# Kernel tuning notes

Hardware: AMD Instinct MI355X
Metric: run time of the kernel (lower is better)

Reference implementation:

```python
import jax, jax.numpy as jnp
import numpy as np

NUM_RELATIONS = 3
NUM_HEADS = 1

N_NODES = 50000
N_EDGES = 300000
D = 256  # in_channels == out_channels == out_channels*num_heads
W_SCALE = 0.02  # realistic init scale; keeps linear-attention normalizer dominated by N_r


def setup_inputs() -> dict:
    key = jax.random.key(0)
    k = jax.random.split(key, 7)
    x = jax.random.normal(k[0], (N_NODES, D), dtype=jnp.float32)
    Wq = jax.random.normal(k[1], (NUM_RELATIONS, D, D * NUM_HEADS), dtype=jnp.float32) * W_SCALE
    Wk = jax.random.normal(k[2], (NUM_RELATIONS, D, D * NUM_HEADS), dtype=jnp.float32) * W_SCALE
    Wv = jax.random.normal(k[3], (NUM_RELATIONS, D, D * NUM_HEADS), dtype=jnp.float32) * W_SCALE
    Whp = jax.random.normal(k[4], (D * NUM_HEADS, D), dtype=jnp.float32) * W_SCALE
    edge_index = jax.random.randint(k[5], (2, N_EDGES), 0, N_NODES, dtype=jnp.int64)
    edge_type = jax.random.randint(k[6], (N_EDGES,), 0, NUM_RELATIONS, dtype=jnp.int64)
    return {"x": x, "Wq": Wq, "Wk": Wk, "Wv": Wv, "Whp": Whp,
            "edge_index": edge_index, "edge_type": edge_type}


def _trans_conv(x, Wq, Wk, Wv, Whp, edge_index, edge_type):
    # x: [N, F], Wq/Wk/Wv: [R, F, H*Dh], Whp: [H*Dh, Dh], edge_index: [2, E]
    row, col = edge_index[0], edge_index[1]
    N = x.shape[0]
    R = Wq.shape[0]
    H = NUM_HEADS
    Dh = Wq.shape[-1] // H
    xr = x[row]  # [E, F] gathered source-node features
    xc = x[col]  # [E, F] gathered target-node features
    x_out = jnp.zeros((N, Dh), dtype=x.dtype)
    for r in range(R):  # small fixed relation loop (structurally distinct weights)
        m = (edge_type == r).astype(x.dtype)  # [E] relation mask (handles ragged sizes)
        Nr = jnp.sum(m)  # number of edges of this relation (the 'N' in full_attention_conv)
        q = (xr @ Wq[r]).reshape(-1, H, Dh)  # [E, H, Dh]
        kk = (xc @ Wk[r]).reshape(-1, H, Dh)
        v = (xc @ Wv[r]).reshape(-1, H, Dh)
        # linear attention (no softmax), masked so only relation-r edges contribute
        kvs = jnp.einsum('e,ehm,ehd->hmd', m, kk, v)        # [H, Dh, Dh]
        num = jnp.einsum('ehm,hmd->ehd', q, kvs) + Nr * v    # [E, H, Dh]
        ks_sum = jnp.einsum('e,ehm->hm', m, kk)              # [H, Dh]
        norm = jnp.einsum('ehm,hm->eh', q, ks_sum)[..., None] + Nr  # [E, H, 1]
        attn = (num / norm).mean(axis=1)                     # [E, Dh] (mean over heads)
        x_out = x_out.at[row].add(m[:, None] * attn)         # scatter-add to source nodes
    return x_out @ Whp  # head projection


def reference(x, Wq, Wk, Wv, Whp, edge_index, edge_type):
    return _trans_conv(x, Wq, Wk, Wv, Whp, edge_index, edge_type)
```

## Files before the change

### kernel.cpp

```cpp
#include <hip/hip_runtime.h>

#define NN 50000
#define EE 300000
#define DD 256
#define RR 3
#define NPAD 50048
#define GS 64
#define SCT (RR * NN)
#define SCB 1024
#define SNB ((SCT + SCB - 1) / SCB)

using bf16x8 = __attribute__((ext_vector_type(8))) short;
using f32x4  = __attribute__((ext_vector_type(4))) float;

__device__ __forceinline__ float bf2f(unsigned short u) {
    return __uint_as_float(((unsigned)u) << 16);
}
__device__ __forceinline__ unsigned short f2bf(float f) {
    unsigned u = __float_as_uint(f);
    return (unsigned short)((u + 0x7fffu + ((u >> 16) & 1u)) >> 16);
}
__device__ __forceinline__ void gload_lds16(const void* g, void* l) {
    __builtin_amdgcn_global_load_lds(
        (const __attribute__((address_space(1))) unsigned int*)g,
        (__attribute__((address_space(3))) unsigned int*)l, 16, 0, 0);
}

__global__ __launch_bounds__(256) void prep_w(
    const float* __restrict__ Wq, const float* __restrict__ Wk,
    const float* __restrict__ Wv, const float* __restrict__ Whp,
    unsigned short* __restrict__ WvTcat, unsigned short* __restrict__ WkT,
    unsigned short* __restrict__ Wqb, unsigned short* __restrict__ WhpT,
    unsigned short* __restrict__ BfullT)
{
    int t = blockIdx.x * 256 + threadIdx.x;
    int slot = t >> 16, o = t & 65535;
    int a = o >> 8, b = o & 255;
    if (slot < 9) {
        int r = slot / 3, kind = slot % 3;
        if (kind == 0)      WvTcat[(size_t)a * 768 + r * 256 + b] = f2bf(Wv[(size_t)r * 65536 + b * 256 + a]);
        else if (kind == 1) WkT[(size_t)r * 65536 + o] = f2bf(Wk[(size_t)r * 65536 + b * 256 + a]);
        else                Wqb[(size_t)r * 65536 + o] = f2bf(Wq[(size_t)r * 65536 + a * 256 + b]);
    } else if (slot == 9) {
        WhpT[o] = f2bf(Whp[b * 256 + a]);
    } else if (slot < 13) {
        int r = slot - 10;
        BfullT[(size_t)768 * 256 + (size_t)r * 65536 + o] = f2bf(Wv[(size_t)r * 65536 + o]);
    }
}

__global__ __launch_bounds__(256) void transpose_conv(
    const float* __restrict__ x, unsigned short* __restrict__ xb,
    unsigned short* __restrict__ xT)
{
    __shared__ unsigned short t[64][66];
    const int n0 = blockIdx.x * 64, i0 = blockIdx.y * 64;
    const int tid = threadIdx.x;
    const int nl = tid >> 2, c0 = (tid & 3) * 16;
    unsigned short vb[16];
    int n = n0 + nl;
    if (n < NN) {
        const float* src = x + (size_t)n * DD + i0 + c0;
#pragma unroll
        for (int q = 0; q < 16; q += 4) {
            float4 v = *(const float4*)(src + q);
            vb[q] = f2bf(v.x); vb[q + 1] = f2bf(v.y);
            vb[q + 2] = f2bf(v.z); vb[q + 3] = f2bf(v.w);
        }
#pragma unroll
        for (int q = 0; q < 16; q += 4)
            *(ushort4*)(xb + (size_t)n * DD + i0 + c0 + q) =
                make_ushort4(vb[q], vb[q + 1], vb[q + 2], vb[q + 3]);
    } else {
#pragma unroll
        for (int q = 0; q < 16; q++) vb[q] = 0;
    }
#pragma unroll
    for (int q = 0; q < 16; q++) t[nl][c0 + q] = vb[q];
    __syncthreads();
    const int il = tid >> 2, nc0 = (tid & 3) * 16;
    unsigned short ob[16];
#pragma unroll
    for (int q = 0; q < 16; q++) ob[q] = t[nc0 + q][il];
#pragma unroll
    for (int q = 0; q < 16; q += 4)
        *(ushort4*)(xT + (size_t)(i0 + il) * NPAD + n0 + nc0 + q) =
            make_ushort4(ob[q], ob[q + 1], ob[q + 2], ob[q + 3]);
}

__global__ __launch_bounds__(256) void count_kernel(
    const int* __restrict__ erow, const int* __restrict__ ecol,
    const int* __restrict__ etype, int* __restrict__ c_in,
    int* __restrict__ c_out, int* __restrict__ nr)
{
    __shared__ int lnr[RR];
    if (threadIdx.x < RR) lnr[threadIdx.x] = 0;
    __syncthreads();
    int g = blockIdx.x * blockDim.x + threadIdx.x;
    int stride = gridDim.x * blockDim.x;
    for (int e = g; e < EE; e += stride) {
        int t = etype[e];
        atomicAdd(&c_out[t * NN + erow[e]], 1);
        atomicAdd(&c_in[t * NN + ecol[e]], 1);
        atomicAdd(&lnr[t], 1);
    }
    __syncthreads();
    if (threadIdx.x < RR) atomicAdd(&nr[threadIdx.x], lnr[threadIdx.x]);
}

__global__ __launch_bounds__(256) void scan_reduce(
    const int* __restrict__ cnt, int* __restrict__ bsum)
{
    __shared__ int ws[4];
    const int b = blockIdx.x, tid = threadIdx.x;
    const int i = b * SCB + tid * 4;
    int s = 0;
    if (i < SCT) {
        int4 v = *(const int4*)(cnt + i);
        s = v.x + v.y + v.z + v.w;
    }
#pragma unroll
    for (int off = 32; off; off >>= 1) s += __shfl_down(s, off, 64);
    if ((tid & 63) == 0) ws[tid >> 6] = s;
    __syncthreads();
    if (tid == 0) bsum[b] = ws[0] + ws[1] + ws[2] + ws[3];
}

__global__ __launch_bounds__(256) void scan_top(
    const int* __restrict__ bsum, int* __restrict__ boff, int* __restrict__ offT)
{
    __shared__ int bs[256];
    const int tid = threadIdx.x;
    int v = tid < SNB ? bsum[tid] : 0;
    bs[tid] = v;
    __syncthreads();
    for (int d = 1; d < 256; d <<= 1) {
        int t = (tid >= d) ? bs[tid - d] : 0;
        __syncthreads();
        bs[tid] += t;
        __syncthreads();
    }
    if (tid < SNB) boff[tid] = tid ? bs[tid - 1] : 0;
    if (tid == 255) *offT = bs[255];
}

__global__ __launch_bounds__(256) void scan_bot(
    const int* __restrict__ cnt, const int* __restrict__ boff,
    int* __restrict__ off, int* __restrict__ cur)
{
    __shared__ int bs[256];
    const int b = blockIdx.x, tid = threadIdx.x;
    const int i = b * SCB + tid * 4;
    int4 v = make_int4(0, 0, 0, 0);
    if (i < SCT) v = *(const int4*)(cnt + i);
    int s = v.x + v.y + v.z + v.w;
    bs[tid] = s;
    __syncthreads();
    for (int d = 1; d < 256; d <<= 1) {
        int t = (tid >= d) ? bs[tid - d] : 0;
        __syncthreads();
        bs[tid] += t;
        __syncthreads();
    }
    if (i < SCT) {
        int pre = boff[b] + (tid ? bs[tid - 1] : 0);
        int4 o;
        o.x = pre;
        o.y = pre + v.x;
        o.z = pre + v.x + v.y;
        o.w = pre + v.x + v.y + v.z;
        *(int4*)(off + i) = o;
        *(int4*)(cur + i) = o;
    }
}

__global__ __launch_bounds__(256) void fill_kernel(
    const int* __restrict__ erow, const int* __restrict__ ecol,
    const int* __restrict__ etype, int* __restrict__ cur,
    int* __restrict__ scol)
{
    int e = blockIdx.x * 256 + threadIdx.x;
    if (e < EE) {
        int key = etype[e] * NN + erow[e];
        int p = atomicAdd(&cur[key], 1);
        scol[p] = ecol[e];
    }
}

__global__ __launch_bounds__(256) void gather_kernel(
    const unsigned short* __restrict__ xb, const int* __restrict__ scol,
    const int* __restrict__ off, const float* __restrict__ qs,
    const int* __restrict__ c_out, const int* __restrict__ nr,
    unsigned short* __restrict__ Afull)
{
    const int wid = threadIdx.x >> 6, lane = threadIdx.x & 63;
    const int n = blockIdx.x * 4 + wid;
    if (n >= NN) return;
    ushort4 xv = *(const ushort4*)(xb + (size_t)n * DD + lane * 4);
    float xf[4] = {bf2f(xv.x), bf2f(xv.y), bf2f(xv.z), bf2f(xv.w)};
#pragma unroll
    for (int t = 0; t < RR; t++) {
        float nrf = (float)nr[t];
        float denom = qs[(size_t)t * NN + n] + nrf;
        int cnt = c_out[t * NN + n];
        float s2 = cnt ? (float)cnt / denom : 0.f;
        ushort4 o1;
        o1.x = f2bf(s2 * xf[0]); o1.y = f2bf(s2 * xf[1]);
        o1.z = f2bf(s2 * xf[2]); o1.w = f2bf(s2 * xf[3]);
        *(ushort4*)(Afull + (size_t)n * 1536 + t * 256 + lane * 4) = o1;

        float acc[4] = {0.f, 0.f, 0.f, 0.f};
        int b0 = off[t * NN + n], b1 = off[t * NN + n + 1];
        for (int i = b0; i < b1; i++) {
            int col = scol[i];
            ushort4 v = *(const ushort4*)(xb + (size_t)col * DD + lane * 4);
            acc[0] += bf2f(v.x); acc[1] += bf2f(v.y);
            acc[2] += bf2f(v.z); acc[3] += bf2f(v.w);
        }
        float s1 = nrf / denom;
        ushort4 o2;
        o2.x = f2bf(s1 * acc[0]); o2.y = f2bf(s1 * acc[1]);
        o2.z = f2bf(s1 * acc[2]); o2.w = f2bf(s1 * acc[3]);
        *(ushort4*)(Afull + (size_t)n * 1536 + 768 + t * 256 + lane * 4) = o2;
    }
}

__global__ __launch_bounds__(256) void wbf_kernel(
    const int* __restrict__ c_in, unsigned short* __restrict__ wbf)
{
    int t = blockIdx.x * 256 + threadIdx.x;
    if (t < 3 * NPAD) {
        int r = t / NPAD, n = t % NPAD;
        wbf[t] = f2bf(n < NN ? (float)c_in[r * NN + n] : 0.f);
    }
}

__global__ __launch_bounds__(256) void xw_kernel(
    const unsigned short* __restrict__ xT, const int* __restrict__ c_in,
    float* __restrict__ xw)
{
    __shared__ float red[3][4];
    const int i = blockIdx.x;
    const int tid = threadIdx.x;
    float a0 = 0.f, a1 = 0.f, a2 = 0.f;
    for (int n = tid * 4; n < NN; n += 1024) {
        ushort4 xv = *(const ushort4*)(xT + (size_t)i * NPAD + n);
        int4 w0 = *(const int4*)(c_in + n);
        int4 w1 = *(const int4*)(c_in + NN + n);
        int4 w2 = *(const int4*)(c_in + 2 * NN + n);
        float f0 = bf2f(xv.x), f1 = bf2f(xv.y), f2 = bf2f(xv.z), f3 = bf2f(xv.w);
        a0 += f0 * w0.x + f1 * w0.y + f2 * w0.z + f3 * w0.w;
        a1 += f0 * w1.x + f1 * w1.y + f2 * w1.z + f3 * w1.w;
        a2 += f0 * w2.x + f1 * w2.y + f2 * w2.z + f3 * w2.w;
    }
#pragma unroll
    for (int off = 32; off; off >>= 1) {
        a0 += __shfl_down(a0, off, 64);
        a1 += __shfl_down(a1, off, 64);
        a2 += __shfl_down(a2, off, 64);
    }
    if ((tid & 63) == 0) {
        red[0][tid >> 6] = a0; red[1][tid >> 6] = a1; red[2][tid >> 6] = a2;
    }
    __syncthreads();
    if (tid < 3)
        xw[tid * 256 + i] = red[tid][0] + red[tid][1] + red[tid][2] + red[tid][3];
}

__global__ __launch_bounds__(512) void g_kernel(
    const unsigned short* __restrict__ xT, const unsigned short* __restrict__ wbf,
    float* __restrict__ Gp)
{
    __shared__ __align__(16) char ldsA[16384];
    __shared__ __align__(16) char ldsB[16384];
    const int tid = threadIdx.x, lane = tid & 63, wid = tid >> 6;
    const int wr = wid >> 1, wc = wid & 1;
    const int i0 = blockIdx.x * 128, j0 = blockIdx.y * 128;
    const int TPZ = (NPAD / 64 + GS - 1) / GS;
    const int kt0 = blockIdx.z * TPZ;
    const int kt1 = min(NPAD / 64, kt0 + TPZ);

    f32x4 acc[3][2][4];
#pragma unroll
    for (int r = 0; r < 3; r++)
#pragma unroll
        for (int m = 0; m < 2; m++)
#pragma unroll
            for (int n = 0; n < 4; n++) acc[r][m][n] = (f32x4){0.f, 0.f, 0.f, 0.f};

    for (int kt = kt0; kt < kt1; kt++) {
        const int kbyte = kt * 128;
#pragma unroll
        for (int is = 0; is < 2; is++) {
            int lb = is * 8192 + wid * 1024;
            int d = lb + lane * 16;
            int row = d >> 7;
            int sc_ = (d & 127) ^ ((row & 7) << 4);
            gload_lds16((const char*)xT + (size_t)(i0 + row) * (NPAD * 2) + kbyte + sc_, ldsA + lb);
            gload_lds16((const char*)xT + (size_t)(j0 + row) * (NPAD * 2) + kbyte + sc_, ldsB + lb);
        }
        __syncthreads();
#pragma unroll
        for (int kk = 0; kk < 2; kk++) {
            const int cb = kk * 64 + ((lane >> 4) << 4);
            bf16x8 bfr[4];
#pragma unroll
            for (int n = 0; n < 4; n++) {
                int rn = wc * 64 + n * 16 + (lane & 15);
                bfr[n] = *(const bf16x8*)(ldsB + rn * 128 + (cb ^ ((rn & 7) << 4)));
            }
            float au[2][8];
#pragma unroll
            for (int m = 0; m < 2; m++) {
                int row = wr * 32 + m * 16 + (lane & 15);
                bf16x8 ar = *(const bf16x8*)(ldsA + row * 128 + (cb ^ ((row & 7) << 4)));
#pragma unroll
                for (int q = 0; q < 8; q++) au[m][q] = bf2f((unsigned short)ar[q]);
            }
            const int nb = kt * 64 + kk * 32 + ((lane >> 4) << 3);
#pragma unroll
            for (int r = 0; r < 3; r++) {
                bf16x8 wv = *(const bf16x8*)(wbf + (size_t)r * NPAD + nb);
                float wf[8];
#pragma unroll
                for (int q = 0; q < 8; q++) wf[q] = bf2f((unsigned short)wv[q]);
                bf16x8 am[2];
#pragma unroll
                for (int m = 0; m < 2; m++)
#pragma unroll
                    for (int q = 0; q < 8; q++)
                        am[m][q] = (short)f2bf(au[m][q] * wf[q]);
#pragma unroll
                for (int m = 0; m < 2; m++)
#pragma unroll
                    for (int n = 0; n < 4; n++)
                        acc[r][m][n] = __builtin_amdgcn_mfma_f32_16x16x32_bf16(
                            am[m], bfr[n], acc[r][m][n], 0, 0, 0);
            }
        }
        __syncthreads();
    }
    float* base = Gp + ((size_t)blockIdx.z * 4 + blockIdx.x * 2 + blockIdx.y) * 3 * 16384;
#pragma unroll
    for (int r = 0; r < 3; r++)
#pragma unroll
        for (int m = 0; m < 2; m++)
#pragma unroll
            for (int n = 0; n < 4; n++) {
                int col = wc * 64 + n * 16 + (lane & 15);
                int rw0 = wr * 32 + m * 16 + ((lane >> 4) << 2);
#pragma unroll
                for (int reg = 0; reg < 4; reg++)
                    base[r * 16384 + (rw0 + reg) * 128 + col] = acc[r][m][n][reg];
            }
}

__global__ __launch_bounds__(256) void greduce_kernel(
    const float* __restrict__ Gp, unsigned short* __restrict__ Gb)
{
    int gid = blockIdx.x * 256 + threadIdx.x;
    int t = gid >> 14, rem = gid & 16383;
    int r = t % 3, tile = t / 3;
    float s = 0.f;
    for (int z = 0; z < GS; z++)
        s += Gp[(size_t)z * 196608 + ((size_t)tile * 3 + r) * 16384 + rem];
    int i = (tile >> 1) * 128 + (rem >> 7);
    int j = (tile & 1) * 128 + (rem & 127);
    Gb[(size_t)r * 65536 + i * 256 + j] = f2bf(s);
}

__global__ __launch_bounds__(256) void matvec_bf(
    const unsigned short* __restrict__ Mat, const float* __restrict__ v,
    float* __restrict__ y)
{
    __shared__ float vs[256];
    const int b = blockIdx.x;
    const int r = b >> 6, rb = (b & 63) * 4;
    const int tid = threadIdx.x;
    vs[tid] = v[r * 256 + tid];
    __syncthreads();
    const int wid = tid >> 6, lane = tid & 63;
    const int row = rb + wid;
    ushort4 m4 = *(const ushort4*)(Mat + (size_t)r * 65536 + row * 256 + lane * 4);
    float s = bf2f(m4.x) * vs[lane * 4] + bf2f(m4.y) * vs[lane * 4 + 1] +
              bf2f(m4.z) * vs[lane * 4 + 2] + bf2f(m4.w) * vs[lane * 4 + 3];
#pragma unroll
    for (int off = 32; off; off >>= 1) s += __shfl_down(s, off, 64);
    if (lane == 0) y[r * 256 + row] = s;
}

__global__ __launch_bounds__(256) void qs_kernel(
    const unsigned short* __restrict__ xb, const float* __restrict__ tv,
    float* __restrict__ qs)
{
    __shared__ float ts[768];
    const int tid = threadIdx.x;
    for (int k = tid; k < 768; k += 256) ts[k] = tv[k];
    __syncthreads();
    const int wid = tid >> 6, lane = tid & 63;
    const int n = blockIdx.x * 4 + wid;
    if (n < NN) {
        ushort4 xv = *(const ushort4*)(xb + (size_t)n * DD + lane * 4);
        float xf[4] = {bf2f(xv.x), bf2f(xv.y), bf2f(xv.z), bf2f(xv.w)};
        float s0 = 0, s1 = 0, s2 = 0;
#pragma unroll
        for (int c = 0; c < 4; c++) {
            s0 += xf[c] * ts[lane * 4 + c];
            s1 += xf[c] * ts[256 + lane * 4 + c];
            s2 += xf[c] * ts[512 + lane * 4 + c];
        }
#pragma unroll
        for (int off = 32; off; off >>= 1) {
            s0 += __shfl_down(s0, off, 64);
            s1 += __shfl_down(s1, off, 64);
            s2 += __shfl_down(s2, off, 64);
        }
        if (lane == 0) { qs[n] = s0; qs[NN + n] = s1; qs[2 * NN + n] = s2; }
    }
}

template <int MODE>
__global__ __launch_bounds__(256) void gemm_nt(
    const unsigned short* __restrict__ A, int lda,
    const unsigned short* __restrict__ B, int ldb,
    void* __restrict__ Cv, int ldc, int M, int KK,
    size_t sa, size_t sb, size_t sc)
{
    A += (size_t)blockIdx.z * sa;
    B += (size_t)blockIdx.z * sb;
    __shared__ __align__(16) char ldsA[16384];
    __shared__ __align__(16) char ldsB[16384];
    const int tid = threadIdx.x, lane = tid & 63, wid = tid >> 6;
    const int wr = wid >> 1, wc = wid & 1;
    const int row0 = blockIdx.x * 128, col0 = blockIdx.y * 128;

    f32x4 acc[4][4];
#pragma unroll
    for (int m = 0; m < 4; m++)
#pragma unroll
        for (int n = 0; n < 4; n++) acc[m][n] = (f32x4){0.f, 0.f, 0.f, 0.f};

    for (int k0 = 0; k0 < KK; k0 += 64) {
#pragma unroll
        for (int is = 0; is < 4; is++) {
            int lb = is * 4096 + wid * 1024;
            int d = lb + lane * 16;
            int row = d >> 7;
            int sc_ = (d & 127) ^ ((row & 7) << 4);
            int gr = row0 + row; gr = gr < M ? gr : M - 1;
            gload_lds16((const char*)(A + (size_t)gr * lda + k0) + sc_, ldsA + lb);
            int rn = col0 + row;
            gload_lds16((const char*)(B + (size_t)rn * ldb + k0) + sc_, ldsB + lb);
        }
        __syncthreads();
#pragma unroll
        for (int kk = 0; kk < 2; kk++) {
            bf16x8 af[4], bf_[4];
            const int cb = kk * 64 + ((lane >> 4) << 4);
#pragma unroll
            for (int m = 0; m < 4; m++) {
                int row = wr * 64 + m * 16 + (lane & 15);
                af[m] = *(const bf16x8*)(ldsA + row * 128 + (cb ^ ((row & 7) << 4)));
                int rn = wc * 64 + m * 16 + (lane & 15);
                bf_[m] = *(const bf16x8*)(ldsB + rn * 128 + (cb ^ ((rn & 7) << 4)));
            }
#pragma unroll
            for (int m = 0; m < 4; m++)
#pragma unroll
                for (int n = 0; n < 4; n++)
                    acc[m][n] = __builtin_amdgcn_mfma_f32_16x16x32_bf16(
                        af[m], bf_[n], acc[m][n], 0, 0, 0);
        }
        __syncthreads();
    }

#pragma unroll
    for (int m = 0; m < 4; m++) {
#pragma unroll
        for (int reg = 0; reg < 4; reg++) {
            int r = row0 + wr * 64 + m * 16 + ((lane >> 4) << 2) + reg;
            if (r >= M) continue;
#pragma unroll
            for (int n = 0; n < 4; n++) {
                int c = col0 + wc * 64 + n * 16 + (lane & 15);
                float v = acc[m][n][reg];
                if (MODE == 0)
                    ((unsigned short*)Cv)[(size_t)blockIdx.z * sc + (size_t)r * ldc + c] = f2bf(v);
                else
                    ((float*)Cv)[(size_t)blockIdx.z * sc + (size_t)r * ldc + c] = v;
            }
        }
    }
}

extern "C" void kernel_launch(void* const* d_in, const int* in_sizes, int n_in,
                              void* d_out, int out_size, void* d_ws, size_t ws_size,
                              hipStream_t stream)
{
    const float* x   = (const float*)d_in[0];
    const float* Wq  = (const float*)d_in[1];
    const float* Wk  = (const float*)d_in[2];
    const float* Wv  = (const float*)d_in[3];
    const float* Whp = (const float*)d_in[4];
    const int* eidx  = (const int*)d_in[5];
    const int* etyp  = (const int*)d_in[6];
    const int* erow = eidx;
    const int* ecol = eidx + EE;
    float* out = (float*)d_out;

    char* p = (char*)d_ws;
    unsigned short* xb    = (unsigned short*)p; p += (size_t)NN * DD * 2;
    unsigned short* xT    = (unsigned short*)p; p += (size_t)DD * NPAD * 2;
    char*           regB  = p;                  p += (size_t)NN * 1536 * 2;
    unsigned short* Gb    = (unsigned short*)p; p += (size_t)RR * 65536 * 2;
    unsigned short* U1    = (unsigned short*)p; p += (size_t)RR * 65536 * 2;
    unsigned short* U2    = (unsigned short*)p; p += (size_t)RR * 65536 * 2;
    unsigned short* BfullT= (unsigned short*)p; p += (size_t)1536 * 256 * 2;
    unsigned short* Bout  = (unsigned short*)p; p += (size_t)256 * 1536 * 2;
    unsigned short* WvTcat= (unsigned short*)p; p += (size_t)256 * 768 * 2;
    unsigned short* WkT   = (unsigned short*)p; p += (size_t)RR * 65536 * 2;
    unsigned short* Wqb   = (unsigned short*)p; p += (size_t)RR * 65536 * 2;
    unsigned short* WhpT  = (unsigned short*)p; p += 65536 * 2;
    unsigned short* wbf   = (unsigned short*)p; p += (size_t)RR * NPAD * 2;
    float*          qs    = (float*)p;          p += (size_t)RR * NN * 4;
    float*          xw    = (float*)p;          p += 768 * 4;
    float*          ks    = (float*)p;          p += 768 * 4;
    float*          tv    = (float*)p;          p += 768 * 4;
    int*            c_in  = (int*)p;            p += (size_t)RR * NN * 4;
    int*            c_out = (int*)p;            p += (size_t)RR * NN * 4;
    int*            off   = (int*)p;            p += (size_t)(RR * NN + 4) * 4;
    int*            cur   = (int*)p;            p += (size_t)RR * NN * 4;
    int*            scol  = (int*)p;            p += (size_t)EE * 4;
    int*            nr    = (int*)p;            p += RR * 4;
    int*            bsum  = (int*)p;            p += SNB * 4;
    int*            boff  = (int*)p;            p += SNB * 4;
    float*          Gp    = (float*)regB;
    unsigned short* Afull = (unsigned short*)regB;

    prep_w<<<3328, 256, 0, stream>>>(Wq, Wk, Wv, Whp, WvTcat, WkT, Wqb, WhpT, BfullT);
    transpose_conv<<<dim3(NPAD / 64, 4), 256, 0, stream>>>(x, xb, xT);
    hipMemsetAsync(c_in, 0, (size_t)(6 * NN) * sizeof(int), stream);
    hipMemsetAsync(nr, 0, RR * sizeof(int), stream);
    count_kernel<<<512, 256, 0, stream>>>(erow, ecol, etyp, c_in, c_out, nr);
    scan_reduce<<<SNB, 256, 0, stream>>>(c_out, bsum);
    scan_top<<<1, 256, 0, stream>>>(bsum, boff, off + SCT);
    scan_bot<<<SNB, 256, 0, stream>>>(c_out, boff, off, cur);
    fill_kernel<<<(EE + 255) / 256, 256, 0, stream>>>(erow, ecol, etyp, cur, scol);
    wbf_kernel<<<(3 * NPAD + 255) / 256, 256, 0, stream>>>(c_in, wbf);
    xw_kernel<<<256, 256, 0, stream>>>(xT, c_in, xw);

    g_kernel<<<dim3(2, 2, GS), 512, 0, stream>>>(xT, wbf, Gp);
    greduce_kernel<<<12 * 64, 256, 0, stream>>>(Gp, Gb);

    gemm_nt<0><<<dim3(2, 2, 3), 256, 0, stream>>>(WvTcat, 768, Gb, 256, U1, 256, 256, 256,
                                                  256, 65536, 65536);
    gemm_nt<0><<<dim3(2, 2, 3), 256, 0, stream>>>(U1, 256, WkT, 256, U2, 256, 256, 256,
                                                  65536, 65536, 65536);
    gemm_nt<0><<<dim3(2, 2, 3), 256, 0, stream>>>(Wqb, 256, U2, 256, BfullT, 256, 256, 256,
                                                  65536, 65536, 65536);
    gemm_nt<0><<<dim3(2, 12), 256, 0, stream>>>(WhpT, 256, BfullT, 256, Bout, 1536, 256, 256,
                                                0, 0, 0);
    matvec_bf<<<192, 256, 0, stream>>>(WkT, xw, ks);
    matvec_bf<<<192, 256, 0, stream>>>(Wqb, ks, tv);
    qs_kernel<<<(NN + 3) / 4, 256, 0, stream>>>(xb, tv, qs);

    gather_kernel<<<(NN + 3) / 4, 256, 0, stream>>>(xb, scol, off, qs, c_out, nr, Afull);

    const int MB = (NN + 127) / 128;
    gemm_nt<1><<<dim3(MB, 2), 256, 0, stream>>>(Afull, 1536, Bout, 1536, out, 256, NN, 1536,
                                                0, 0, 0);
}
```

Before: 341.1 us.

## Fuse prep kernels, reassociate small weight GEMM chain, fold qs into gather, swizzle GEMM

Merges weight conversion and x transpose/convert into one launch, and merges the wbf and xw kernels. It reassociates the small weight-product chain: Wq·Wk^T is formed once and reused for both the Gram-based term and the normalizer vector, dropping one 256x256 GEMM and one matvec. It also folds the per-node qs dot products into the gather kernel, removing a kernel and the qs buffer round trip. The final big GEMM gets an XCD-aware block swizzle for better L2 locality. Together these cut launch count and small serial kernels, but the reordered bf16 intermediate products may change rounding.

```diff
diff --git a/kernel.cpp b/kernel.cpp
--- a/kernel.cpp
+++ b/kernel.cpp
@@ -9,6 +9,7 @@
 #define SCT (RR * NN)
 #define SCB 1024
 #define SNB ((SCT + SCB - 1) / SCB)
+#define TBLK 3128
 
 using bf16x8 = __attribute__((ext_vector_type(8))) short;
 using f32x4  = __attribute__((ext_vector_type(4))) float;
@@ -26,66 +27,58 @@
         (__attribute__((address_space(3))) unsigned int*)l, 16, 0, 0);
 }
 
-__global__ __launch_bounds__(256) void prep_w(
-    const float* __restrict__ Wq, const float* __restrict__ Wk,
-    const float* __restrict__ Wv, const float* __restrict__ Whp,
-    unsigned short* __restrict__ WvTcat, unsigned short* __restrict__ WkT,
-    unsigned short* __restrict__ Wqb, unsigned short* __restrict__ WhpT,
-    unsigned short* __restrict__ BfullT)
-{
-    int t = blockIdx.x * 256 + threadIdx.x;
-    int slot = t >> 16, o = t & 65535;
-    int a = o >> 8, b = o & 255;
-    if (slot < 9) {
-        int r = slot / 3, kind = slot % 3;
-        if (kind == 0)      WvTcat[(size_t)a * 768 + r * 256 + b] = f2bf(Wv[(size_t)r * 65536 + b * 256 + a]);
-        else if (kind == 1) WkT[(size_t)r * 65536 + o] = f2bf(Wk[(size_t)r * 65536 + b * 256 + a]);
-        else                Wqb[(size_t)r * 65536 + o] = f2bf(Wq[(size_t)r * 65536 + a * 256 + b]);
-    } else if (slot == 9) {
-        WhpT[o] = f2bf(Whp[b * 256 + a]);
-    } else if (slot < 13) {
-        int r = slot - 10;
-        BfullT[(size_t)768 * 256 + (size_t)r * 65536 + o] = f2bf(Wv[(size_t)r * 65536 + o]);
-    }
-}
-
-__global__ __launch_bounds__(256) void transpose_conv(
-    const float* __restrict__ x, unsigned short* __restrict__ xb,
-    unsigned short* __restrict__ xT)
-{
-    __shared__ unsigned short t[64][66];
-    const int n0 = blockIdx.x * 64, i0 = blockIdx.y * 64;
+__global__ __launch_bounds__(256) void prep_tc(
+    const float* __restrict__ x, const float* __restrict__ Wq,
+    const float* __restrict__ Wk, const float* __restrict__ Wv,
+    const float* __restrict__ Whp,
+    unsigned short* __restrict__ xb, unsigned short* __restrict__ xT,
+    unsigned short* __restrict__ Wqb, unsigned short* __restrict__ Wkb,
+    unsigned short* __restrict__ Wvb, unsigned short* __restrict__ WhpT)
+{
     const int tid = threadIdx.x;
-    const int nl = tid >> 2, c0 = (tid & 3) * 16;
-    unsigned short vb[16];
-    int n = n0 + nl;
-    if (n < NN) {
-        const float* src = x + (size_t)n * DD + i0 + c0;
-#pragma unroll
-        for (int q = 0; q < 16; q += 4) {
-            float4 v = *(const float4*)(src + q);
-            vb[q] = f2bf(v.x); vb[q + 1] = f2bf(v.y);
-            vb[q + 2] = f2bf(v.z); vb[q + 3] = f2bf(v.w);
-        }
+    if (blockIdx.x < TBLK) {
+        __shared__ unsigned short t[64][66];
+        const int tb = blockIdx.x;
+        const int n0 = (tb % 782) * 64, i0 = (tb / 782) * 64;
+        const int nl = tid >> 2, c0 = (tid & 3) * 16;
+        unsigned short vb[16];
+        int n = n0 + nl;
+        if (n < NN) {
+            const float* src = x + (size_t)n * DD + i0 + c0;
+#pragma unroll
+            for (int q = 0; q < 16; q += 4) {
+                float4 v = *(const float4*)(src + q);
+                vb[q] = f2bf(v.x); vb[q + 1] = f2bf(v.y);
+                vb[q + 2] = f2bf(v.z); vb[q + 3] = f2bf(v.w);
+            }
+#pragma unroll
+            for (int q = 0; q < 16; q += 4)
+                *(ushort4*)(xb + (size_t)n * DD + i0 + c0 + q) =
+                    make_ushort4(vb[q], vb[q + 1], vb[q + 2], vb[q + 3]);
+        } else {
+#pragma unroll
+            for (int q = 0; q < 16; q++) vb[q] = 0;
+        }
+#pragma unroll
+        for (int q = 0; q < 16; q++) t[nl][c0 + q] = vb[q];
+        __syncthreads();
+        const int il = tid >> 2, nc0 = (tid & 3) * 16;
+        unsigned short ob[16];
+#pragma unroll
+        for (int q = 0; q < 16; q++) ob[q] = t[nc0 + q][il];
 #pragma unroll
         for (int q = 0; q < 16; q += 4)
-            *(ushort4*)(xb + (size_t)n * DD + i0 + c0 + q) =
-                make_ushort4(vb[q], vb[q + 1], vb[q + 2], vb[q + 3]);
+            *(ushort4*)(xT + (size_t)(i0 + il) * NPAD + n0 + nc0 + q) =
+                make_ushort4(ob[q], ob[q + 1], ob[q + 2], ob[q + 3]);
     } else {
-#pragma unroll
-        for (int q = 0; q < 16; q++) vb[q] = 0;
-    }
-#pragma unroll
-    for (int q = 0; q < 16; q++) t[nl][c0 + q] = vb[q];
-    __syncthreads();
-    const int il = tid >> 2, nc0 = (tid & 3) * 16;
-    unsigned short ob[16];
-#pragma unroll
-    for (int q = 0; q < 16; q++) ob[q] = t[nc0 + q][il];
-#pragma unroll
-    for (int q = 0; q < 16; q += 4)
-        *(ushort4*)(xT + (size_t)(i0 + il) * NPAD + n0 + nc0 + q) =
-            make_ushort4(ob[q], ob[q + 1], ob[q + 2], ob[q + 3]);
+        int t = (blockIdx.x - TBLK) * 256 + tid;
+        int slot = t >> 16, o = t & 65535;
+        int a = o >> 8, b = o & 255;
+        if (slot < 3)       Wqb[(size_t)slot * 65536 + o] = f2bf(Wq[(size_t)slot * 65536 + o]);
+        else if (slot < 6)  Wkb[(size_t)(slot - 3) * 65536 + o] = f2bf(Wk[(size_t)(slot - 3) * 65536 + o]);
+        else if (slot < 9)  Wvb[(size_t)(slot - 6) * 65536 + o] = f2bf(Wv[(size_t)(slot - 6) * 65536 + o]);
+        else if (slot == 9) WhpT[o] = f2bf(Whp[b * 256 + a]);
+    }
 }
 
 __global__ __launch_bounds__(256) void count_kernel(
@@ -187,84 +180,44 @@
     }
 }
 
-__global__ __launch_bounds__(256) void gather_kernel(
-    const unsigned short* __restrict__ xb, const int* __restrict__ scol,
-    const int* __restrict__ off, const float* __restrict__ qs,
-    const int* __restrict__ c_out, const int* __restrict__ nr,
-    unsigned short* __restrict__ Afull)
-{
-    const int wid = threadIdx.x >> 6, lane = threadIdx.x & 63;
-    const int n = blockIdx.x * 4 + wid;
-    if (n >= NN) return;
-    ushort4 xv = *(const ushort4*)(xb + (size_t)n * DD + lane * 4);
-    float xf[4] = {bf2f(xv.x), bf2f(xv.y), bf2f(xv.z), bf2f(xv.w)};
-#pragma unroll
-    for (int t = 0; t < RR; t++) {
-        float nrf = (float)nr[t];
-        float denom = qs[(size_t)t * NN + n] + nrf;
-        int cnt = c_out[t * NN + n];
-        float s2 = cnt ? (float)cnt / denom : 0.f;
-        ushort4 o1;
-        o1.x = f2bf(s2 * xf[0]); o1.y = f2bf(s2 * xf[1]);
-        o1.z = f2bf(s2 * xf[2]); o1.w = f2bf(s2 * xf[3]);
-        *(ushort4*)(Afull + (size_t)n * 1536 + t * 256 + lane * 4) = o1;
-
-        float acc[4] = {0.f, 0.f, 0.f, 0.f};
-        int b0 = off[t * NN + n], b1 = off[t * NN + n + 1];
-        for (int i = b0; i < b1; i++) {
-            int col = scol[i];
-            ushort4 v = *(const ushort4*)(xb + (size_t)col * DD + lane * 4);
-            acc[0] += bf2f(v.x); acc[1] += bf2f(v.y);
-            acc[2] += bf2f(v.z); acc[3] += bf2f(v.w);
-        }
-        float s1 = nrf / denom;
-        ushort4 o2;
-        o2.x = f2bf(s1 * acc[0]); o2.y = f2bf(s1 * acc[1]);
-        o2.z = f2bf(s1 * acc[2]); o2.w = f2bf(s1 * acc[3]);
-        *(ushort4*)(Afull + (size_t)n * 1536 + 768 + t * 256 + lane * 4) = o2;
-    }
-}
-
-__global__ __launch_bounds__(256) void wbf_kernel(
-    const int* __restrict__ c_in, unsigned short* __restrict__ wbf)
-{
-    int t = blockIdx.x * 256 + threadIdx.x;
-    if (t < 3 * NPAD) {
-        int r = t / NPAD, n = t % NPAD;
-        wbf[t] = f2bf(n < NN ? (float)c_in[r * NN + n] : 0.f);
-    }
-}
-
-__global__ __launch_bounds__(256) void xw_kernel(
+__global__ __launch_bounds__(256) void wbfxw_kernel(
     const unsigned short* __restrict__ xT, const int* __restrict__ c_in,
-    float* __restrict__ xw)
-{
-    __shared__ float red[3][4];
-    const int i = blockIdx.x;
+    float* __restrict__ xw, unsigned short* __restrict__ wbf)
+{
     const int tid = threadIdx.x;
-    float a0 = 0.f, a1 = 0.f, a2 = 0.f;
-    for (int n = tid * 4; n < NN; n += 1024) {
-        ushort4 xv = *(const ushort4*)(xT + (size_t)i * NPAD + n);
-        int4 w0 = *(const int4*)(c_in + n);
-        int4 w1 = *(const int4*)(c_in + NN + n);
-        int4 w2 = *(const int4*)(c_in + 2 * NN + n);
-        float f0 = bf2f(xv.x), f1 = bf2f(xv.y), f2 = bf2f(xv.z), f3 = bf2f(xv.w);
-        a0 += f0 * w0.x + f1 * w0.y + f2 * w0.z + f3 * w0.w;
-        a1 += f0 * w1.x + f1 * w1.y + f2 * w1.z + f3 * w1.w;
-        a2 += f0 * w2.x + f1 * w2.y + f2 * w2.z + f3 * w2.w;
-    }
-#pragma unroll
-    for (int off = 32; off; off >>= 1) {
-        a0 += __shfl_down(a0, off, 64);
-        a1 += __shfl_down(a1, off, 64);
-        a2 += __shfl_down(a2, off, 64);
-    }
-    if ((tid & 63) == 0) {
-        red[0][tid >> 6] = a0; red[1][tid >> 6] = a1; red[2][tid >> 6] = a2;
-    }
-    __syncthreads();
-    if (tid < 3)
-        xw[tid * 256 + i] = red[tid][0] + red[tid][1] + red[tid][2] + red[tid][3];
+    if (blockIdx.x < 256) {
+        __shared__ float red[3][4];
+        const int i = blockIdx.x;
+        float a0 = 0.f, a1 = 0.f, a2 = 0.f;
+        for (int n = tid * 4; n < NN; n += 1024) {
+            ushort4 xv = *(const ushort4*)(xT + (size_t)i * NPAD + n);
+            int4 w0 = *(const int4*)(c_in + n);
+            int4 w1 = *(const int4*)(c_in + NN + n);
+            int4 w2 = *(const int4*)(c_in + 2 * NN + n);
+            float f0 = bf2f(xv.x), f1 = bf2f(xv.y), f2 = bf2f(xv.z), f3 = bf2f(xv.w);
+            a0 += f0 * w0.x + f1 * w0.y + f2 * w0.z + f3 * w0.w;
+            a1 += f0 * w1.x + f1 * w1.y + f2 * w1.z + f3 * w1.w;
+            a2 += f0 * w2.x + f1 * w2.y + f2 * w2.z + f3 * w2.w;
+        }
+#pragma unroll
+        for (int off = 32; off; off >>= 1) {
+            a0 += __shfl_down(a0, off, 64);
+            a1 += __shfl_down(a1, off, 64);
+            a2 += __shfl_down(a2, off, 64);
+        }
+        if ((tid & 63) == 0) {
+            red[0][tid >> 6] = a0; red[1][tid >> 6] = a1; red[2][tid >> 6] = a2;
+        }
+        __syncthreads();
+        if (tid < 3)
+            xw[tid * 256 + i] = red[tid][0] + red[tid][1] + red[tid][2] + red[tid][3];
+    } else {
+        int t = (blockIdx.x - 256) * 256 + tid;
+        if (t < 3 * NPAD) {
+            int r = t / NPAD, n = t % NPAD;
+            wbf[t] = f2bf(n < NN ? (float)c_in[r * NN + n] : 0.f);
+        }
+    }
 }
 
 __global__ __launch_bounds__(512) void g_kernel(
@@ -389,37 +342,60 @@
     if (lane == 0) y[r * 256 + row] = s;
 }
 
-__global__ __launch_bounds__(256) void qs_kernel(
-    const unsigned short* __restrict__ xb, const float* __restrict__ tv,
-    float* __restrict__ qs)
+__global__ __launch_bounds__(256) void gather_kernel(
+    const unsigned short* __restrict__ xb, const int* __restrict__ scol,
+    const int* __restrict__ off, const float* __restrict__ tv,
+    const int* __restrict__ c_out, const int* __restrict__ nr,
+    unsigned short* __restrict__ Afull)
 {
     __shared__ float ts[768];
+    __shared__ float nrs[RR];
     const int tid = threadIdx.x;
     for (int k = tid; k < 768; k += 256) ts[k] = tv[k];
+    if (tid < RR) nrs[tid] = (float)nr[tid];
     __syncthreads();
     const int wid = tid >> 6, lane = tid & 63;
     const int n = blockIdx.x * 4 + wid;
-    if (n < NN) {
-        ushort4 xv = *(const ushort4*)(xb + (size_t)n * DD + lane * 4);
-        float xf[4] = {bf2f(xv.x), bf2f(xv.y), bf2f(xv.z), bf2f(xv.w)};
-        float s0 = 0, s1 = 0, s2 = 0;
-#pragma unroll
-        for (int c = 0; c < 4; c++) {
-            s0 += xf[c] * ts[lane * 4 + c];
-            s1 += xf[c] * ts[256 + lane * 4 + c];
-            s2 += xf[c] * ts[512 + lane * 4 + c];
-        }
-#pragma unroll
-        for (int off = 32; off; off >>= 1) {
-            s0 += __shfl_down(s0, off, 64);
-            s1 += __shfl_down(s1, off, 64);
-            s2 += __shfl_down(s2, off, 64);
-        }
-        if (lane == 0) { qs[n] = s0; qs[NN + n] = s1; qs[2 * NN + n] = s2; }
-    }
-}
-
-template <int MODE>
+    if (n >= NN) return;
+    ushort4 xv = *(const ushort4*)(xb + (size_t)n * DD + lane * 4);
+    float xf[4] = {bf2f(xv.x), bf2f(xv.y), bf2f(xv.z), bf2f(xv.w)};
+    float dots[RR];
+#pragma unroll
+    for (int t = 0; t < RR; t++) {
+        float s = xf[0] * ts[t * 256 + lane * 4] + xf[1] * ts[t * 256 + lane * 4 + 1] +
+                  xf[2] * ts[t * 256 + lane * 4 + 2] + xf[3] * ts[t * 256 + lane * 4 + 3];
+#pragma unroll
+        for (int o = 32; o; o >>= 1) s += __shfl_xor(s, o, 64);
+        dots[t] = s;
+    }
+#pragma unroll
+    for (int t = 0; t < RR; t++) {
+        float nrf = nrs[t];
+        float denom = dots[t] + nrf;
+        int cnt = c_out[t * NN + n];
+        float s2 = cnt ? (float)cnt / denom : 0.f;
+        ushort4 o1;
+        o1.x = f2bf(s2 * xf[0]); o1.y = f2bf(s2 * xf[1]);
+        o1.z = f2bf(s2 * xf[2]); o1.w = f2bf(s2 * xf[3]);
+        *(ushort4*)(Afull + (size_t)n * 1536 + t * 256 + lane * 4) = o1;
+
+        float acc[4] = {0.f, 0.f, 0.f, 0.f};
+        int b0 = off[t * NN + n], b1 = off[t * NN + n + 1];
+        for (int i = b0; i < b1; i++) {
+            int col = scol[i];
+            ushort4 v = *(const ushort4*)(xb + (size_t)col * DD + lane * 4);
+            acc[0] += bf2f(v.x); acc[1] += bf2f(v.y);
+            acc[2] += bf2f(v.z); acc[3] += bf2f(v.w);
+        }
+        float s1 = nrf / denom;
+        ushort4 o2;
+        o2.x = f2bf(s1 * acc[0]); o2.y = f2bf(s1 * acc[1]);
+        o2.z = f2bf(s1 * acc[2]); o2.w = f2bf(s1 * acc[3]);
+        *(ushort4*)(Afull + (size_t)n * 1536 + 768 + t * 256 + lane * 4) = o2;
+    }
+}
+
+template <int MODE, int SWZ>
 __global__ __launch_bounds__(256) void gemm_nt(
     const unsigned short* __restrict__ A, int lda,
     const unsigned short* __restrict__ B, int ldb,
@@ -432,7 +408,13 @@
     __shared__ __align__(16) char ldsB[16384];
     const int tid = threadIdx.x, lane = tid & 63, wid = tid >> 6;
     const int wr = wid >> 1, wc = wid & 1;
-    const int row0 = blockIdx.x * 128, col0 = blockIdx.y * 128;
+    int bx = blockIdx.x;
+    if (SWZ) {
+        int nwg = gridDim.x, q = nwg >> 3, rem = nwg & 7;
+        int xcd = bx & 7, idx = bx >> 3;
+        bx = (xcd < rem ? xcd * (q + 1) : rem * (q + 1) + (xcd - rem) * q) + idx;
+    }
+    const int row0 = bx * 128, col0 = blockIdx.y * 128;
 
     f32x4 acc[4][4];
 #pragma unroll
@@ -513,60 +495,53 @@
     unsigned short* xT    = (unsigned short*)p; p += (size_t)DD * NPAD * 2;
     char*           regB  = p;                  p += (size_t)NN * 1536 * 2;
     unsigned short* Gb    = (unsigned short*)p; p += (size_t)RR * 65536 * 2;
-    unsigned short* U1    = (unsigned short*)p; p += (size_t)RR * 65536 * 2;
-    unsigned short* U2    = (unsigned short*)p; p += (size_t)RR * 65536 * 2;
-    unsigned short* BfullT= (unsigned short*)p; p += (size_t)1536 * 256 * 2;
+    unsigned short* M1    = (unsigned short*)p; p += (size_t)RR * 65536 * 2;
+    unsigned short* Tm    = (unsigned short*)p; p += (size_t)RR * 65536 * 2;
     unsigned short* Bout  = (unsigned short*)p; p += (size_t)256 * 1536 * 2;
-    unsigned short* WvTcat= (unsigned short*)p; p += (size_t)256 * 768 * 2;
-    unsigned short* WkT   = (unsigned short*)p; p += (size_t)RR * 65536 * 2;
     unsigned short* Wqb   = (unsigned short*)p; p += (size_t)RR * 65536 * 2;
+    unsigned short* Wkb   = (unsigned short*)p; p += (size_t)RR * 65536 * 2;
+    unsigned short* Wvb   = (unsigned short*)p; p += (size_t)RR * 65536 * 2;
     unsigned short* WhpT  = (unsigned short*)p; p += 65536 * 2;
     unsigned short* wbf   = (unsigned short*)p; p += (size_t)RR * NPAD * 2;
-    float*          qs    = (float*)p;          p += (size_t)RR * NN * 4;
     float*          xw    = (float*)p;          p += 768 * 4;
-    float*          ks    = (float*)p;          p += 768 * 4;
     float*          tv    = (float*)p;          p += 768 * 4;
     int*            c_in  = (int*)p;            p += (size_t)RR * NN * 4;
     int*            c_out = (int*)p;            p += (size_t)RR * NN * 4;
+    int*            nr    = (int*)p;            p += 4 * 4;
     int*            off   = (int*)p;            p += (size_t)(RR * NN + 4) * 4;
     int*            cur   = (int*)p;            p += (size_t)RR * NN * 4;
     int*            scol  = (int*)p;            p += (size_t)EE * 4;
-    int*            nr    = (int*)p;            p += RR * 4;
     int*            bsum  = (int*)p;            p += SNB * 4;
     int*            boff  = (int*)p;            p += SNB * 4;
     float*          Gp    = (float*)regB;
     unsigned short* Afull = (unsigned short*)regB;
 
-    prep_w<<<3328, 256, 0, stream>>>(Wq, Wk, Wv, Whp, WvTcat, WkT, Wqb, WhpT, BfullT);
-    transpose_conv<<<dim3(NPAD / 64, 4), 256, 0, stream>>>(x, xb, xT);
-    hipMemsetAsync(c_in, 0, (size_t)(6 * NN) * sizeof(int), stream);
-    hipMemsetAsync(nr, 0, RR * sizeof(int), stream);
+    prep_tc<<<TBLK + 2560, 256, 0, stream>>>(x, Wq, Wk, Wv, Whp, xb, xT, Wqb, Wkb, Wvb, WhpT);
+    hipMemsetAsync(c_in, 0, (size_t)(6 * NN + 4) * sizeof(int), stream);
     count_kernel<<<512, 256, 0, stream>>>(erow, ecol, etyp, c_in, c_out, nr);
     scan_reduce<<<SNB, 256, 0, stream>>>(c_out, bsum);
     scan_top<<<1, 256, 0, stream>>>(bsum, boff, off + SCT);
     scan_bot<<<SNB, 256, 0, stream>>>(c_out, boff, off, cur);
     fill_kernel<<<(EE + 255) / 256, 256, 0, stream>>>(erow, ecol, etyp, cur, scol);
-    wbf_kernel<<<(3 * NPAD + 255) / 256, 256, 0, stream>>>(c_in, wbf);
-    xw_kernel<<<256, 256, 0, stream>>>(xT, c_in, xw);
+    wbfxw_kernel<<<256 + (3 * NPAD + 255) / 256, 256, 0, stream>>>(xT, c_in, xw, wbf);
+
+    gemm_nt<0, 0><<<dim3(2, 2, 3), 256, 0, stream>>>(Wqb, 256, Wkb, 256, M1, 256, 256, 256,
+                                                     65536, 65536, 65536);
+    gemm_nt<0, 0><<<dim3(2, 2, 3), 256, 0, stream>>>(WhpT, 256, Wvb, 256, Bout + 768, 1536,
+                                                     256, 256, 0, 65536, 256);
 
     g_kernel<<<dim3(2, 2, GS), 512, 0, stream>>>(xT, wbf, Gp);
     greduce_kernel<<<12 * 64, 256, 0, stream>>>(Gp, Gb);
 
-    gemm_nt<0><<<dim3(2, 2, 3), 256, 0, stream>>>(WvTcat, 768, Gb, 256, U1, 256, 256, 256,
-                                                  256, 65536, 65536);
-    gemm_nt<0><<<dim3(2, 2, 3), 256, 0, stream>>>(U1, 256, WkT, 256, U2, 256, 256, 256,
-                                                  65536, 65536, 65536);
-    gemm_nt<0><<<dim3(2, 2, 3), 256, 0, stream>>>(Wqb, 256, U2, 256, BfullT, 256, 256, 256,
-                                                  65536, 65536, 65536);
-    gemm_nt<0><<<dim3(2, 12), 256, 0, stream>>>(WhpT, 256, BfullT, 256, Bout, 1536, 256, 256,
-                                                0, 0, 0);
-    matvec_bf<<<192, 256, 0, stream>>>(WkT, xw, ks);
-    matvec_bf<<<192, 256, 0, stream>>>(Wqb, ks, tv);
-    qs_kernel<<<(NN + 3) / 4, 256, 0, stream>>>(xb, tv, qs);
-
-    gather_kernel<<<(NN + 3) / 4, 256, 0, stream>>>(xb, scol, off, qs, c_out, nr, Afull);
+    gemm_nt<0, 0><<<dim3(2, 2, 3), 256, 0, stream>>>(M1, 256, Gb, 256, Tm, 256, 256, 256,
+                                                     65536, 65536, 65536);
+    gemm_nt<0, 0><<<dim3(2, 2, 3), 256, 0, stream>>>(Bout + 768, 1536, Tm, 256, Bout, 1536,
+                                                     256, 256, 256, 65536, 256);
+    matvec_bf<<<192, 256, 0, stream>>>(M1, xw, tv);
+
+    gather_kernel<<<(NN + 3) / 4, 256, 0, stream>>>(xb, scol, off, tv, c_out, nr, Afull);
 
     const int MB = (NN + 127) / 128;
-    gemm_nt<1><<<dim3(MB, 2), 256, 0, stream>>>(Afull, 1536, Bout, 1536, out, 256, NN, 1536,
-                                                0, 0, 0);
-}
+    gemm_nt<1, 1><<<dim3(MB, 2), 256, 0, stream>>>(Afull, 1536, Bout, 1536, out, 256, NN, 1536,
+                                                   0, 0, 0);
+}
```

After: 320.2 us. 1.07x faster.
